# Optimization experiments

Hardware: AMD Instinct MI355X
Metric: run time of the kernel (lower is better)

The kernel has to match this reference:

```python
import jax, jax.numpy as jnp
import numpy as np

D_MODEL = 512
N_HEADS = 8
D_K = D_MODEL // N_HEADS


def setup_inputs() -> dict:
    key = jax.random.key(0)
    k1, k2, k3 = jax.random.split(key, 3)
    x = jax.random.normal(k1, (2, 4096, D_MODEL), dtype=jnp.float32)
    # torch Linear weights: [out, in]; we store transposed [in, out] for x @ W
    s_qkv = 1.0 / np.sqrt(D_MODEL)
    W_qkv = jax.random.uniform(k2, (D_MODEL, 3 * D_MODEL), dtype=jnp.float32, minval=-s_qkv, maxval=s_qkv)
    W_out = jax.random.uniform(k3, (D_MODEL, D_MODEL), dtype=jnp.float32, minval=-s_qkv, maxval=s_qkv)
    return {"x": x, "W_qkv": W_qkv, "W_out": W_out}


def reference(x, W_qkv, W_out):
    B, S, _ = x.shape
    qkv = (x @ W_qkv).reshape(B, S, 3, N_HEADS, D_K)
    q, k, v = qkv[:, :, 0], qkv[:, :, 1], qkv[:, :, 2]  # [B,S,H,Dk]
    scale = 1.0 / np.sqrt(D_K).astype(np.float32)
    scores = jnp.einsum('bshd,bthd->bhst', q, k) * scale  # [B,H,S,S]
    attn = jax.nn.softmax(scores, axis=-1)
    out = jnp.einsum('bhst,bthd->bshd', attn, v).reshape(B, S, D_MODEL)
    return out @ W_out
```

## Files before the change

### kernel.cpp

```cpp
#include <hip/hip_runtime.h>
#include <hip/hip_bf16.h>

#define SEQ 4096
#define NB 2
#define DM 512
#define NH 8
#define DK 64

typedef __bf16 bf16;
typedef __bf16 bf16x4 __attribute__((ext_vector_type(4)));
typedef __bf16 bf16x8 __attribute__((ext_vector_type(8)));
typedef float  f32x4 __attribute__((ext_vector_type(4)));

__device__ __forceinline__ f32x4 mfma16(bf16x8 a, bf16x8 b, f32x4 c) {
    return __builtin_amdgcn_mfma_f32_16x16x32_bf16(a, b, c, 0, 0, 0);
}

__device__ __forceinline__ float fexp2(float x) {
    return __builtin_amdgcn_exp2f(x);
}

__device__ __forceinline__ void gload_lds16(const bf16* g, bf16* l) {
    __builtin_amdgcn_global_load_lds(
        (const __attribute__((address_space(1))) void*)g,
        (__attribute__((address_space(3))) void*)l, 16, 0, 0);
}

__device__ __forceinline__ int swzE(int row, int e) {
    return row * 64 + (e ^ ((row & 7) << 3));
}

__device__ __forceinline__ bf16x8 cvt8(const float* __restrict__ p) {
    const float4 v0 = *(const float4*)p;
    const float4 v1 = *(const float4*)(p + 4);
    return (bf16x8){(bf16)v0.x, (bf16)v0.y, (bf16)v0.z, (bf16)v0.w,
                    (bf16)v1.x, (bf16)v1.y, (bf16)v1.z, (bf16)v1.w};
}

__global__ __launch_bounds__(256)
void prep_w(const float* __restrict__ W, bf16* __restrict__ Wth, int K, int N) {
    __shared__ float T[64][65];
    const int k0 = blockIdx.x * 64, n0 = blockIdx.y * 64;
    const int t = threadIdx.x;
    #pragma unroll
    for (int i = 0; i < 4; ++i) {
        int r = i * 16 + (t >> 4);
        int c = (t & 15) * 4;
        float4 v = *(const float4*)&W[(size_t)(k0 + r) * N + n0 + c];
        T[r][c + 0] = v.x; T[r][c + 1] = v.y; T[r][c + 2] = v.z; T[r][c + 3] = v.w;
    }
    __syncthreads();
    #pragma unroll
    for (int i = 0; i < 4; ++i) {
        int n = i * 16 + (t >> 4);
        int c = (t & 15) * 4;
        bf16x4 hv = (bf16x4){(bf16)T[c + 0][n], (bf16)T[c + 1][n],
                             (bf16)T[c + 2][n], (bf16)T[c + 3][n]};
        *(bf16x4*)&Wth[(size_t)(n0 + n) * K + k0 + c] = hv;
    }
}

template<int FUSE>
__global__ __launch_bounds__(256, 2)
void gemm_bf16(const float* __restrict__ A, const bf16* __restrict__ Bth,
               float* __restrict__ C,
               bf16* __restrict__ Qout, bf16* __restrict__ Kout,
               bf16* __restrict__ Vout, int M, int N, int K) {
    __shared__ __align__(16) char smem_raw[36864];
    bf16* Ah = (bf16*)smem_raw;
    bf16* Bh = Ah + 128 * 64;

    const int t = threadIdx.x;
    const int lane = t & 63, w = t >> 6;
    const int l15 = lane & 15, g = lane >> 4;
    const int wm = (w >> 1) * 64, wn = (w & 1) * 64;
    const int rowA = blockIdx.y * 128;
    const int colB = blockIdx.x * 128;
    const int sr = t >> 1;
    const int sc = (t & 1) * 32;

    f32x4 acc[4][4] = {};

    for (int k0 = 0; k0 < K; k0 += 64) {
        __syncthreads();
        #pragma unroll
        for (int u = 0; u < 4; ++u) {
            int off = swzE(sr, sc + u * 8);
            *(bf16x8*)&Ah[off] = cvt8(&A[(size_t)(rowA + sr) * K + k0 + sc + u * 8]);
        }
        #pragma unroll
        for (int u = 0; u < 4; ++u) {
            int off = swzE(sr, sc + u * 8);
            *(bf16x8*)&Bh[off] = *(const bf16x8*)&Bth[(size_t)(colB + sr) * K + k0 + sc + u * 8];
        }
        __syncthreads();
        #pragma unroll
        for (int kst = 0; kst < 2; ++kst) {
            bf16x8 ah[4];
            #pragma unroll
            for (int mi = 0; mi < 4; ++mi) {
                int off = swzE(wm + mi * 16 + l15, kst * 32 + g * 8);
                ah[mi] = *(const bf16x8*)&Ah[off];
            }
            #pragma unroll
            for (int ni = 0; ni < 4; ++ni) {
                int off = swzE(wn + ni * 16 + l15, kst * 32 + g * 8);
                bf16x8 bh = *(const bf16x8*)&Bh[off];
                #pragma unroll
                for (int mi = 0; mi < 4; ++mi)
                    acc[mi][ni] = mfma16(ah[mi], bh, acc[mi][ni]);
            }
        }
    }

    if (FUSE == 0) {
        #pragma unroll
        for (int mi = 0; mi < 4; ++mi)
            #pragma unroll
            for (int ni = 0; ni < 4; ++ni)
                #pragma unroll
                for (int r = 0; r < 4; ++r) {
                    int row = rowA + wm + mi * 16 + g * 4 + r;
                    int col = colB + wn + ni * 16 + l15;
                    C[(size_t)row * N + col] = acc[mi][ni][r];
                }
    } else {
        const int sec = colB >> 9;
        const float scl = (sec == 0) ? 0.125f * 1.44269504088896f : 1.0f;
        bf16* TB = (bf16*)smem_raw;
        __syncthreads();
        #pragma unroll
        for (int mi = 0; mi < 4; ++mi)
            #pragma unroll
            for (int ni = 0; ni < 4; ++ni)
                #pragma unroll
                for (int r = 0; r < 4; ++r) {
                    const int rr = wm + mi * 16 + g * 4 + r;
                    const int cr = wn + ni * 16 + l15;
                    const float v = acc[mi][ni][r] * scl;
                    if (sec < 2) {
                        TB[rr * 136 + cr] = (bf16)v;
                    } else {
                        const int kk = rr & 63;
                        const int nn = kk >> 4;
                        const int sl = ((nn & 1) << 5) | (((kk >> 2) & 3) << 3)
                                     | ((nn >> 1) << 2) | (kk & 3);
                        TB[cr * 136 + (rr >> 6) * 64 + sl] = (bf16)v;
                    }
                }
        __syncthreads();
        const int b_ = rowA >> 12;
        const int sbase = rowA & 4095;
        #pragma unroll
        for (int pass = 0; pass < 8; ++pass) {
            const int rowi = pass * 16 + (t >> 4);
            const int e8 = (t & 15) * 8;
            bf16x8 v = *(const bf16x8*)&TB[rowi * 136 + e8];
            if (sec < 2) {
                const int ckv = (colB & 511) + e8;
                const int h_ = ckv >> 6, d8 = ckv & 63;
                bf16* dst = (sec == 0) ? Qout : Kout;
                *(bf16x8*)&dst[(((size_t)b_ * NH + h_) * SEQ + sbase + rowi) * DK + d8] = v;
            } else {
                const int cv = (colB - 1024) + rowi;
                const int h_ = cv >> 6, d_ = cv & 63;
                *(bf16x8*)&Vout[(((size_t)b_ * NH + h_) * DK + d_) * SEQ + sbase + e8] = v;
            }
        }
    }
}

__global__ __launch_bounds__(512)
void flash_mfma(const bf16* __restrict__ Qh,
                const bf16* __restrict__ Kh, const bf16* __restrict__ Vth,
                float* __restrict__ att) {
    extern __shared__ bf16 smem[];
    bf16* KhS = smem;
    bf16* VhS = smem + 8192;

    const int nwg = (int)gridDim.x;
    const int cpx = nwg >> 3;
    const int bid = (int)blockIdx.x;
    const int wg = (bid & 7) * cpx + (bid >> 3);
    const int qt = wg & 31;
    const int bh = wg >> 5;

    const int t = threadIdx.x, lane = t & 63, w = t >> 6;
    const int l15 = lane & 15, g = lane >> 4;
    const int q0 = qt * 128;
    const int wq = w * 16;

    bf16x8 qh[2];
    {
        const size_t qbase = ((size_t)bh * SEQ + q0 + wq + l15) * DK + g * 8;
        qh[0] = *(const bf16x8*)&Qh[qbase];
        qh[1] = *(const bf16x8*)&Qh[qbase + 32];
    }

    const bf16 one = (bf16)1.0f;
    const bf16x8 ones = (bf16x8){one, one, one, one, one, one, one, one};

    f32x4 o[4] = {};
    f32x4 lacc = {0.f, 0.f, 0.f, 0.f};

    const int sr = t >> 3;
    const int sc8 = (t & 7) * 8;
    const int scs = sc8 ^ ((sr & 7) << 3);
    const size_t kgo = ((size_t)bh * SEQ + sr) * DK + scs;
    const size_t vgo = ((size_t)bh * DK + sr) * SEQ + scs;
    const int dst = t * 8;

    auto stage = [&](int kt, int c) {
        const int cb = c * 4096 + dst;
        gload_lds16(Kh + kgo + (size_t)kt * 64 * DK, KhS + cb);
        gload_lds16(Vth + vgo + (size_t)kt * 64,     VhS + cb);
    };

    const int NT = SEQ / 64;
    stage(0, 0);
    __syncthreads();

    for (int kt = 0; kt < NT; ++kt) {
        const int c = kt & 1;
        if (kt + 1 < NT) stage(kt + 1, c ^ 1);
        const int cb = c * 4096;

        f32x4 s[4] = {};
        __builtin_amdgcn_s_setprio(1);
        #pragma unroll
        for (int kst = 0; kst < 2; ++kst) {
            #pragma unroll
            for (int ni = 0; ni < 4; ++ni) {
                int off = cb + swzE(ni * 16 + l15, kst * 32 + g * 8);
                bf16x8 kh_ = *(const bf16x8*)&KhS[off];
                s[ni] = mfma16(kh_, qh[kst], s[ni]);
            }
        }
        __builtin_amdgcn_s_setprio(0);

        bf16x8 pa[2];
        #pragma unroll
        for (int ni = 0; ni < 4; ++ni)
            #pragma unroll
            for (int r = 0; r < 4; ++r)
                pa[ni & 1][(ni >> 1) * 4 + r] = (bf16)fexp2(s[ni][r]);

        __builtin_amdgcn_s_setprio(1);
        #pragma unroll
        for (int kst = 0; kst < 2; ++kst) {
            #pragma unroll
            for (int ni = 0; ni < 4; ++ni) {
                int off = cb + swzE(ni * 16 + l15, kst * 32 + g * 8);
                bf16x8 vh_ = *(const bf16x8*)&VhS[off];
                o[ni] = mfma16(pa[kst], vh_, o[ni]);
            }
            lacc = mfma16(pa[kst], ones, lacc);
        }
        __builtin_amdgcn_s_setprio(0);

        __syncthreads();
    }

    const int b = bh >> 3, h = bh & 7;
    #pragma unroll
    for (int r = 0; r < 4; ++r) {
        const float inv = 1.0f / lacc[r];
        const int row = q0 + wq + g * 4 + r;
        #pragma unroll
        for (int ni = 0; ni < 4; ++ni)
            att[(size_t)(b * SEQ + row) * DM + h * DK + ni * 16 + l15] =
                o[ni][r] * inv;
    }
}

extern "C" void kernel_launch(void* const* d_in, const int* in_sizes, int n_in,
                              void* d_out, int out_size, void* d_ws, size_t ws_size,
                              hipStream_t stream) {
    const float* x    = (const float*)d_in[0];
    const float* Wqkv = (const float*)d_in[1];
    const float* Wout = (const float*)d_in[2];
    float* out = (float*)d_out;

    char* ws = (char*)d_ws;
    float* attn = (float*)(ws + (size_t)48 * 1048576);
    bf16* Qhp  = (bf16*)(ws);
    bf16* Khp  = (bf16*)(ws + (size_t)64 * 1048576);
    bf16* Vthp = (bf16*)(ws + (size_t)80 * 1048576);
    bf16* Wqh  = (bf16*)(ws + (size_t)96 * 1048576);
    bf16* Woh  = (bf16*)(ws + (size_t)100 * 1048576);

    const int M = NB * SEQ;
    const int FLASH_LDS = 32768;

    hipFuncSetAttribute((const void*)flash_mfma,
                        hipFuncAttributeMaxDynamicSharedMemorySize, FLASH_LDS);

    prep_w<<<dim3(DM / 64, (3 * DM) / 64), 256, 0, stream>>>(Wqkv, Wqh, DM, 3 * DM);
    prep_w<<<dim3(DM / 64, DM / 64), 256, 0, stream>>>(Wout, Woh, DM, DM);

    gemm_bf16<1><<<dim3((3 * DM) / 128, M / 128), 256, 0, stream>>>(
        x, Wqh, nullptr, Qhp, Khp, Vthp, M, 3 * DM, DM);

    flash_mfma<<<dim3((SEQ / 128) * NH * NB), 512, FLASH_LDS, stream>>>(
        Qhp, Khp, Vthp, attn);

    gemm_bf16<0><<<dim3(DM / 128, M / 128), 256, 0, stream>>>(
        attn, Woh, out, nullptr, nullptr, nullptr, M, DM, DM);
}
```

Baseline: 141.6 us.

## Store attention output as bf16 and merge weight prep kernels

The flash kernel now writes its attention output in bf16 instead of fp32. A dedicated output-projection GEMM reads that bf16 directly, so it no longer converts fp32 activations on load. This halves the intermediate write and read traffic. The two weight-transpose launches are also merged into one kernel to save a launch. The output GEMM uses a simple synchronous LDS staging path, and the extra rounding of the attention output is a small precision cost.

```diff
diff --git a/kernel.cpp b/kernel.cpp
--- a/kernel.cpp
+++ b/kernel.cpp
@@ -38,10 +38,15 @@
 }
 
 __global__ __launch_bounds__(256)
-void prep_w(const float* __restrict__ W, bf16* __restrict__ Wth, int K, int N) {
+void prep_w2(const float* __restrict__ Wqkv, const float* __restrict__ Wout,
+             bf16* __restrict__ Wqh, bf16* __restrict__ Woh) {
     __shared__ float T[64][65];
-    const int k0 = blockIdx.x * 64, n0 = blockIdx.y * 64;
     const int t = threadIdx.x;
+    const int bx = blockIdx.x, by = blockIdx.y;
+    const float* W; bf16* D; int N, n0;
+    if (by < 24) { W = Wqkv; D = Wqh; N = 3 * DM; n0 = by * 64; }
+    else         { W = Wout; D = Woh; N = DM;     n0 = (by - 24) * 64; }
+    const int k0 = bx * 64;
     #pragma unroll
     for (int i = 0; i < 4; ++i) {
         int r = i * 16 + (t >> 4);
@@ -56,16 +61,14 @@
         int c = (t & 15) * 4;
         bf16x4 hv = (bf16x4){(bf16)T[c + 0][n], (bf16)T[c + 1][n],
                              (bf16)T[c + 2][n], (bf16)T[c + 3][n]};
-        *(bf16x4*)&Wth[(size_t)(n0 + n) * K + k0 + c] = hv;
-    }
-}
-
-template<int FUSE>
+        *(bf16x4*)&D[(size_t)(n0 + n) * DM + k0 + c] = hv;
+    }
+}
+
 __global__ __launch_bounds__(256, 2)
-void gemm_bf16(const float* __restrict__ A, const bf16* __restrict__ Bth,
-               float* __restrict__ C,
-               bf16* __restrict__ Qout, bf16* __restrict__ Kout,
-               bf16* __restrict__ Vout, int M, int N, int K) {
+void gemm_qkv(const float* __restrict__ A, const bf16* __restrict__ Bth,
+              bf16* __restrict__ Qout, bf16* __restrict__ Kout,
+              bf16* __restrict__ Vout, int M, int N, int K) {
     __shared__ __align__(16) char smem_raw[36864];
     bf16* Ah = (bf16*)smem_raw;
     bf16* Bh = Ah + 128 * 64;
@@ -113,67 +116,109 @@
         }
     }
 
-    if (FUSE == 0) {
-        #pragma unroll
-        for (int mi = 0; mi < 4; ++mi)
-            #pragma unroll
-            for (int ni = 0; ni < 4; ++ni)
+    const int sec = colB >> 9;
+    const float scl = (sec == 0) ? 0.125f * 1.44269504088896f : 1.0f;
+    bf16* TB = (bf16*)smem_raw;
+    __syncthreads();
+    #pragma unroll
+    for (int mi = 0; mi < 4; ++mi)
+        #pragma unroll
+        for (int ni = 0; ni < 4; ++ni)
+            #pragma unroll
+            for (int r = 0; r < 4; ++r) {
+                const int rr = wm + mi * 16 + g * 4 + r;
+                const int cr = wn + ni * 16 + l15;
+                const float v = acc[mi][ni][r] * scl;
+                if (sec < 2) {
+                    TB[rr * 136 + cr] = (bf16)v;
+                } else {
+                    const int kk = rr & 63;
+                    const int nn = kk >> 4;
+                    const int sl = ((nn & 1) << 5) | (((kk >> 2) & 3) << 3)
+                                 | ((nn >> 1) << 2) | (kk & 3);
+                    TB[cr * 136 + (rr >> 6) * 64 + sl] = (bf16)v;
+                }
+            }
+    __syncthreads();
+    const int b_ = rowA >> 12;
+    const int sbase = rowA & 4095;
+    #pragma unroll
+    for (int pass = 0; pass < 8; ++pass) {
+        const int rowi = pass * 16 + (t >> 4);
+        const int e8 = (t & 15) * 8;
+        bf16x8 v = *(const bf16x8*)&TB[rowi * 136 + e8];
+        if (sec < 2) {
+            const int ckv = (colB & 511) + e8;
+            const int h_ = ckv >> 6, d8 = ckv & 63;
+            bf16* dst = (sec == 0) ? Qout : Kout;
+            *(bf16x8*)&dst[(((size_t)b_ * NH + h_) * SEQ + sbase + rowi) * DK + d8] = v;
+        } else {
+            const int cv = (colB - 1024) + rowi;
+            const int h_ = cv >> 6, d_ = cv & 63;
+            *(bf16x8*)&Vout[(((size_t)b_ * NH + h_) * DK + d_) * SEQ + sbase + e8] = v;
+        }
+    }
+}
+
+__global__ __launch_bounds__(256, 2)
+void gemm_out(const bf16* __restrict__ A, const bf16* __restrict__ Bth,
+              float* __restrict__ C, int M, int N, int K) {
+    __shared__ __align__(16) bf16 Ah[128 * 64], Bh[128 * 64];
+
+    const int t = threadIdx.x;
+    const int lane = t & 63, w = t >> 6;
+    const int l15 = lane & 15, g = lane >> 4;
+    const int wm = (w >> 1) * 64, wn = (w & 1) * 64;
+    const int rowA = blockIdx.y * 128;
+    const int colB = blockIdx.x * 128;
+    const int sr = t >> 1;
+    const int sc = (t & 1) * 32;
+
+    f32x4 acc[4][4] = {};
+
+    for (int k0 = 0; k0 < K; k0 += 64) {
+        __syncthreads();
+        #pragma unroll
+        for (int u = 0; u < 4; ++u) {
+            int off = swzE(sr, sc + u * 8);
+            *(bf16x8*)&Ah[off] = *(const bf16x8*)&A[(size_t)(rowA + sr) * K + k0 + sc + u * 8];
+            *(bf16x8*)&Bh[off] = *(const bf16x8*)&Bth[(size_t)(colB + sr) * K + k0 + sc + u * 8];
+        }
+        __syncthreads();
+        #pragma unroll
+        for (int kst = 0; kst < 2; ++kst) {
+            bf16x8 ah[4];
+            #pragma unroll
+            for (int mi = 0; mi < 4; ++mi) {
+                int off = swzE(wm + mi * 16 + l15, kst * 32 + g * 8);
+                ah[mi] = *(const bf16x8*)&Ah[off];
+            }
+            #pragma unroll
+            for (int ni = 0; ni < 4; ++ni) {
+                int off = swzE(wn + ni * 16 + l15, kst * 32 + g * 8);
+                bf16x8 bh = *(const bf16x8*)&Bh[off];
                 #pragma unroll
-                for (int r = 0; r < 4; ++r) {
-                    int row = rowA + wm + mi * 16 + g * 4 + r;
-                    int col = colB + wn + ni * 16 + l15;
-                    C[(size_t)row * N + col] = acc[mi][ni][r];
-                }
-    } else {
-        const int sec = colB >> 9;
-        const float scl = (sec == 0) ? 0.125f * 1.44269504088896f : 1.0f;
-        bf16* TB = (bf16*)smem_raw;
-        __syncthreads();
-        #pragma unroll
-        for (int mi = 0; mi < 4; ++mi)
-            #pragma unroll
-            for (int ni = 0; ni < 4; ++ni)
-                #pragma unroll
-                for (int r = 0; r < 4; ++r) {
-                    const int rr = wm + mi * 16 + g * 4 + r;
-                    const int cr = wn + ni * 16 + l15;
-                    const float v = acc[mi][ni][r] * scl;
-                    if (sec < 2) {
-                        TB[rr * 136 + cr] = (bf16)v;
-                    } else {
-                        const int kk = rr & 63;
-                        const int nn = kk >> 4;
-                        const int sl = ((nn & 1) << 5) | (((kk >> 2) & 3) << 3)
-                                     | ((nn >> 1) << 2) | (kk & 3);
-                        TB[cr * 136 + (rr >> 6) * 64 + sl] = (bf16)v;
-                    }
-                }
-        __syncthreads();
-        const int b_ = rowA >> 12;
-        const int sbase = rowA & 4095;
-        #pragma unroll
-        for (int pass = 0; pass < 8; ++pass) {
-            const int rowi = pass * 16 + (t >> 4);
-            const int e8 = (t & 15) * 8;
-            bf16x8 v = *(const bf16x8*)&TB[rowi * 136 + e8];
-            if (sec < 2) {
-                const int ckv = (colB & 511) + e8;
-                const int h_ = ckv >> 6, d8 = ckv & 63;
-                bf16* dst = (sec == 0) ? Qout : Kout;
-                *(bf16x8*)&dst[(((size_t)b_ * NH + h_) * SEQ + sbase + rowi) * DK + d8] = v;
-            } else {
-                const int cv = (colB - 1024) + rowi;
-                const int h_ = cv >> 6, d_ = cv & 63;
-                *(bf16x8*)&Vout[(((size_t)b_ * NH + h_) * DK + d_) * SEQ + sbase + e8] = v;
-            }
-        }
-    }
+                for (int mi = 0; mi < 4; ++mi)
+                    acc[mi][ni] = mfma16(ah[mi], bh, acc[mi][ni]);
+            }
+        }
+    }
+    #pragma unroll
+    for (int mi = 0; mi < 4; ++mi)
+        #pragma unroll
+        for (int ni = 0; ni < 4; ++ni)
+            #pragma unroll
+            for (int r = 0; r < 4; ++r) {
+                int row = rowA + wm + mi * 16 + g * 4 + r;
+                int col = colB + wn + ni * 16 + l15;
+                C[(size_t)row * N + col] = acc[mi][ni][r];
+            }
 }
 
 __global__ __launch_bounds__(512)
 void flash_mfma(const bf16* __restrict__ Qh,
                 const bf16* __restrict__ Kh, const bf16* __restrict__ Vth,
-                float* __restrict__ att) {
+                bf16* __restrict__ att) {
     extern __shared__ bf16 smem[];
     bf16* KhS = smem;
     bf16* VhS = smem + 8192;
@@ -269,7 +314,7 @@
         #pragma unroll
         for (int ni = 0; ni < 4; ++ni)
             att[(size_t)(b * SEQ + row) * DM + h * DK + ni * 16 + l15] =
-                o[ni][r] * inv;
+                (bf16)(o[ni][r] * inv);
     }
 }
 
@@ -282,8 +327,8 @@
     float* out = (float*)d_out;
 
     char* ws = (char*)d_ws;
-    float* attn = (float*)(ws + (size_t)48 * 1048576);
     bf16* Qhp  = (bf16*)(ws);
+    bf16* attn = (bf16*)(ws + (size_t)48 * 1048576);
     bf16* Khp  = (bf16*)(ws + (size_t)64 * 1048576);
     bf16* Vthp = (bf16*)(ws + (size_t)80 * 1048576);
     bf16* Wqh  = (bf16*)(ws + (size_t)96 * 1048576);
@@ -295,15 +340,14 @@
     hipFuncSetAttribute((const void*)flash_mfma,
                         hipFuncAttributeMaxDynamicSharedMemorySize, FLASH_LDS);
 
-    prep_w<<<dim3(DM / 64, (3 * DM) / 64), 256, 0, stream>>>(Wqkv, Wqh, DM, 3 * DM);
-    prep_w<<<dim3(DM / 64, DM / 64), 256, 0, stream>>>(Wout, Woh, DM, DM);
-
-    gemm_bf16<1><<<dim3((3 * DM) / 128, M / 128), 256, 0, stream>>>(
-        x, Wqh, nullptr, Qhp, Khp, Vthp, M, 3 * DM, DM);
+    prep_w2<<<dim3(DM / 64, 32), 256, 0, stream>>>(Wqkv, Wout, Wqh, Woh);
+
+    gemm_qkv<<<dim3((3 * DM) / 128, M / 128), 256, 0, stream>>>(
+        x, Wqh, Qhp, Khp, Vthp, M, 3 * DM, DM);
 
     flash_mfma<<<dim3((SEQ / 128) * NH * NB), 512, FLASH_LDS, stream>>>(
         Qhp, Khp, Vthp, attn);
 
-    gemm_bf16<0><<<dim3(DM / 128, M / 128), 256, 0, stream>>>(
-        attn, Woh, out, nullptr, nullptr, nullptr, M, DM, DM);
-}
+    gemm_out<<<dim3(DM / 128, M / 128), 256, 0, stream>>>(
+        attn, Woh, out, M, DM, DM);
+}
```

After: 132.4 us. 1.07x faster.
